# Optimization experiments

Hardware: AMD Instinct MI355X
Metric: run time of the kernel (lower is better)

The kernel has to match this reference:

```python
import jax, jax.numpy as jnp
import numpy as np

REL, DIM = 8, 256
B, S, T = 8, 512, 512


def setup_inputs() -> dict:
    key = jax.random.key(0)
    k = jax.random.split(key, 8)
    return {
        "src_emb": jax.random.normal(k[0], (B, S, DIM), jnp.float32),
        "tar_emb": jax.random.normal(k[1], (B, T, DIM), jnp.float32),
        "src_mask": jnp.ones((B, S), jnp.float32),
        "tar_mask": jnp.ones((B, T), jnp.float32),
        "mul_score_w": jax.random.normal(k[2], (REL, DIM, DIM), jnp.float32) * 0.05,
        "mul_emb_w": jax.random.normal(k[3], (REL, DIM, DIM), jnp.float32) * 0.05,
        "src_none_node": jax.random.normal(k[4], (DIM,), jnp.float32),
        "tar_none_node": jax.random.normal(k[5], (DIM,), jnp.float32),
    }


def reference(src_emb, tar_emb, src_mask, tar_mask,
              mul_score_w, mul_emb_w, src_none_node, tar_none_node):
    b = src_emb.shape[0]
    dim = src_emb.shape[2]
    rel = mul_score_w.shape[0]
    ones = jnp.ones((b, 1), src_mask.dtype)
    # append learned 'none' node to both src and tar (always unmasked)
    src_mask_ = jnp.concatenate([src_mask, ones], axis=1)            # [b, S+1]
    src_emb_ = jnp.concatenate(
        [src_emb, jnp.broadcast_to(src_none_node[None, None, :], (b, 1, dim))], axis=1)
    tar_mask_ = jnp.concatenate([tar_mask, ones], axis=1)            # [b, T+1]
    tar_emb_ = jnp.concatenate(
        [tar_emb, jnp.broadcast_to(tar_none_node[None, None, :], (b, 1, dim))], axis=1)

    # per-relation projected src: [rel, b, S+1, dim]
    scores = jnp.einsum('bsd,rde->rbse', src_emb_, mul_score_w)
    # relation-wise bilinear scores: [rel, b, S+1, T+1]
    st = jnp.einsum('rbse,bte->rbst', scores, tar_emb_)
    pair_mask = src_mask_[:, :, None] * tar_mask_[:, None, :]        # [b, S+1, T+1]
    st = (st + (1.0 - pair_mask)[None] * (-1e10)) * (1.0 / np.sqrt(dim))
    # softmax over the SRC axis (softmax_src=True)
    w = jax.nn.softmax(st, axis=2)                                   # [rel, b, S+1, T+1]

    # per-relation projected tar: [rel, b, T+1, dim]
    rel_tar = jnp.einsum('btd,rde->rbte', tar_emb_, mul_emb_w)
    # use_tar_node=False: drop appended tar none-node from both factors
    rel_tar = rel_tar[:, :, :-1, :]                                  # [rel, b, T, dim]
    w = w[:, :, :, :-1]                                              # [rel, b, S+1, T]

    # tar_sum=True, use_normalize=False: sum over tar then rel, scaled by 1/sqrt(rel)
    mul_emb = jnp.einsum('rbst,rbtd->bsd', w, rel_tar) * (1.0 / np.sqrt(rel))
    # src_none_node present: drop appended src row
    return mul_emb[:, :-1, :]                                        # [b, S, dim]
```

## Files before the change

### kernel.cpp

```cpp
#include <hip/hip_runtime.h>

#define RELN 8
#define DIMN 256
#define BN_  8
#define SN   512
#define TN   512

typedef __attribute__((ext_vector_type(8))) short bf16x8;
typedef __attribute__((ext_vector_type(4))) short bf16x4;
typedef __attribute__((ext_vector_type(4))) float f32x4;

__device__ __forceinline__ unsigned short f2bf(float f) {
    union { float f; unsigned u; } x; x.f = f;
    return (unsigned short)((x.u + 0x7FFFu + ((x.u >> 16) & 1u)) >> 16);
}
__device__ __forceinline__ float bf2f(unsigned short h) {
    union { unsigned u; float f; } x; x.u = (unsigned)h << 16; return x.f;
}

#define TBM 128
#define TBN 128
#define TBK 64
#define BP  132

template<int MODE>
__global__ __launch_bounds__(256, 2)
void gemm_bt(const unsigned short* __restrict__ A,
             const unsigned short* __restrict__ B,
             void* __restrict__ C, int K, int lda, int ldb,
             const float* __restrict__ msrc,
             const float* __restrict__ mtar,
             float* __restrict__ Lsum)
{
    __shared__ unsigned short Sh[2][2][TBM * TBK];
    const int tid  = threadIdx.x;
    const int lane = tid & 63;
    const int wv   = tid >> 6;
    const int wr   = (wv >> 1) * 64;
    const int wc   = (wv & 1) * 64;
    const int m0   = blockIdx.x * TBM;
    const int n0   = blockIdx.y * TBN;
    const int z    = blockIdx.z;
    const int bblk = m0 >> 9;
    const int rz   = z * 2;

    const unsigned short* Ab = A;
    const unsigned short* Bb = B;
    if (MODE == 1)      { Bb += (size_t)z * DIMN * DIMN; }
    else if (MODE == 2) { Ab += (size_t)z * SN * DIMN; Bb += (size_t)(z & 7) * TN * DIMN; }
    else if (MODE == 3) { Bb += (size_t)z * DIMN * DIMN; }

    auto stage = [&](int buf, int kt) {
        #pragma unroll
        for (int p = 0; p < 4; ++p) {
            int idx8 = p * 256 + tid;
            int row  = idx8 >> 3;
            int col  = (idx8 & 7) << 3;
            size_t aoff, boff;
            if (MODE == 4) {
                int r = rz + (kt >> 9);
                int t = (kt & 511) + col;
                aoff = ((size_t)((r*BN_ + bblk)*SN + ((m0 + row) & 511)))*TN + t;
                boff = ((size_t)((r*BN_ + bblk)*DIMN + (n0 + row)))*TN + t;
            } else {
                aoff = (size_t)(m0 + row)*lda + kt + col;
                boff = (size_t)(n0 + row)*ldb + kt + col;
            }
            __builtin_amdgcn_global_load_lds(
                (const __attribute__((address_space(1))) unsigned int*)&Ab[aoff],
                (__attribute__((address_space(3))) unsigned int*)
                    &Sh[buf][0][p*2048 + wv*512], 16, 0, 0);
            __builtin_amdgcn_global_load_lds(
                (const __attribute__((address_space(1))) unsigned int*)&Bb[boff],
                (__attribute__((address_space(3))) unsigned int*)
                    &Sh[buf][1][p*2048 + wv*512], 16, 0, 0);
        }
    };

    f32x4 acc[4][4] = {};
    const int nsteps = K / TBK;
    stage(0, 0);
    int cur = 0;
    for (int s = 0; s < nsteps; ++s) {
        __syncthreads();
        if (s + 1 < nsteps) stage(cur ^ 1, (s + 1) * TBK);
        const unsigned short* As = Sh[cur][0];
        const unsigned short* Bs = Sh[cur][1];
        #pragma unroll
        for (int kk = 0; kk < 2; ++kk) {
            const int ko = kk*32 + (lane >> 4) * 8;
            bf16x8 af[4], bfv[4];
            #pragma unroll
            for (int i = 0; i < 4; ++i)
                af[i] = *(const bf16x8*)&As[(wr + i*16 + (lane & 15))*TBK + ko];
            #pragma unroll
            for (int j = 0; j < 4; ++j)
                bfv[j] = *(const bf16x8*)&Bs[(wc + j*16 + (lane & 15))*TBK + ko];
            #pragma unroll
            for (int i = 0; i < 4; ++i) {
                #pragma unroll
                for (int j = 0; j < 4; ++j)
                    acc[i][j] = __builtin_amdgcn_mfma_f32_16x16x32_bf16(af[i], bfv[j], acc[i][j], 0, 0, 0);
            }
        }
        cur ^= 1;
    }

    const int r0 = (lane >> 4) * 4;
    const int cl = lane & 15;
    unsigned short* tile = &Sh[0][0][0];

    if (MODE == 2) {
        unsigned short* Cp = (unsigned short*)C + (size_t)z * SN * TN;
        const int b = z & 7;
        float tm[4];
        #pragma unroll
        for (int j = 0; j < 4; ++j) tm[j] = mtar[b*TN + n0 + wc + j*16 + cl];
        float colsum[4] = {0.f, 0.f, 0.f, 0.f};
        __syncthreads();
        #pragma unroll
        for (int i = 0; i < 4; ++i) {
            int rowl = wr + i*16 + r0;
            float sm[4];
            #pragma unroll
            for (int q = 0; q < 4; ++q) sm[q] = msrc[b*SN + m0 + rowl + q];
            #pragma unroll
            for (int j = 0; j < 4; ++j) {
                int coll = wc + j*16 + cl;
                #pragma unroll
                for (int q = 0; q < 4; ++q) {
                    float v = (acc[i][j][q] + (1.f - sm[q]*tm[j]) * -1e10f) * 0.0625f;
                    float e = __expf(v);
                    tile[(rowl + q)*BP + coll] = f2bf(e);
                    colsum[j] += e;
                }
            }
        }
        #pragma unroll
        for (int j = 0; j < 4; ++j) {
            float v = colsum[j];
            v += __shfl_xor(v, 16, 64);
            v += __shfl_xor(v, 32, 64);
            if (lane < 16)
                atomicAdd(&Lsum[(size_t)z*TN + n0 + wc + j*16 + cl], v);
        }
        __syncthreads();
        #pragma unroll
        for (int p = 0; p < 8; ++p) {
            int chunk = p * 256 + tid;
            int row = chunk >> 4, col = (chunk & 15) * 8;
            bf16x8 v = *(const bf16x8*)&tile[row*BP + col];
            *(bf16x8*)&Cp[(size_t)(m0 + row)*TN + n0 + col] = v;
        }
    } else if (MODE == 1) {
        unsigned short* Cp = (unsigned short*)C + (size_t)z * (BN_*SN) * DIMN;
        __syncthreads();
        #pragma unroll
        for (int i = 0; i < 4; ++i) {
            int rowl = wr + i*16 + r0;
            #pragma unroll
            for (int j = 0; j < 4; ++j) {
                int coll = wc + j*16 + cl;
                #pragma unroll
                for (int q = 0; q < 4; ++q)
                    tile[(rowl + q)*BP + coll] = f2bf(acc[i][j][q]);
            }
        }
        __syncthreads();
        #pragma unroll
        for (int p = 0; p < 8; ++p) {
            int chunk = p * 256 + tid;
            int row = chunk >> 4, col = (chunk & 15) * 8;
            bf16x8 v = *(const bf16x8*)&tile[row*BP + col];
            *(bf16x8*)&Cp[(size_t)(m0 + row)*DIMN + n0 + col] = v;
        }
    } else if (MODE == 3) {
        unsigned short* Cp = (unsigned short*)C;
        #pragma unroll
        for (int i = 0; i < 4; ++i) {
            int mrow = m0 + wr + i*16 + r0;
            int b = mrow >> 9, t = mrow & 511;
            float4 Lv = *(const float4*)&Lsum[((size_t)(z*BN_ + b))*TN + t];
            float inv0 = 1.f / Lv.x, inv1 = 1.f / Lv.y,
                  inv2 = 1.f / Lv.z, inv3 = 1.f / Lv.w;
            #pragma unroll
            for (int j = 0; j < 4; ++j) {
                int e = n0 + wc + j*16 + cl;
                bf16x4 v;
                v[0] = (short)f2bf(acc[i][j][0] * inv0);
                v[1] = (short)f2bf(acc[i][j][1] * inv1);
                v[2] = (short)f2bf(acc[i][j][2] * inv2);
                v[3] = (short)f2bf(acc[i][j][3] * inv3);
                *(bf16x4*)&Cp[((size_t)(z*BN_ + b)*DIMN + e)*TN + t] = v;
            }
        }
    } else {
        float* Cp = (float*)C + (size_t)z * (BN_*SN) * DIMN;
        #pragma unroll
        for (int i = 0; i < 4; ++i) {
            int row = m0 + wr + i*16 + r0;
            #pragma unroll
            for (int j = 0; j < 4; ++j) {
                int col = n0 + wc + j*16 + cl;
                #pragma unroll
                for (int q = 0; q < 4; ++q)
                    Cp[(size_t)(row + q)*DIMN + col] = acc[i][j][q];
            }
        }
    }
}

__global__ void reduce4_kernel(const float* __restrict__ part,
                               float* __restrict__ out, int n4)
{
    int i = blockIdx.x * 256 + threadIdx.x;
    if (i < n4) {
        float4 s = {0.f, 0.f, 0.f, 0.f};
        #pragma unroll
        for (int r = 0; r < 4; ++r) {
            float4 v = *(const float4*)&part[(size_t)r*(BN_*SN*DIMN) + i*4];
            s.x += v.x; s.y += v.y; s.z += v.z; s.w += v.w;
        }
        const float k = 0.35355339059327373f;
        float4 o = {s.x*k, s.y*k, s.z*k, s.w*k};
        *(float4*)&out[i*4] = o;
    }
}

__global__ void cvt2_kernel(const float* __restrict__ src,
                            const float* __restrict__ tar,
                            unsigned short* __restrict__ src_bf,
                            unsigned short* __restrict__ tar_bf)
{
    int bid = blockIdx.x;
    const float* in = (bid < 1024) ? src : tar;
    unsigned short* out = (bid < 1024) ? src_bf : tar_bf;
    int i = ((bid & 1023) * 256 + threadIdx.x) * 4;
    float4 v = *(const float4*)(in + i);
    bf16x4 o;
    o[0] = (short)f2bf(v.x); o[1] = (short)f2bf(v.y);
    o[2] = (short)f2bf(v.z); o[3] = (short)f2bf(v.w);
    *(bf16x4*)(out + i) = o;
}

__global__ void wtrans2_kernel(const float* __restrict__ wsc,
                               const float* __restrict__ wem,
                               unsigned short* __restrict__ wscT,
                               unsigned short* __restrict__ wembT)
{
    __shared__ float tile[32][33];
    int r = blockIdx.z & 7;
    const float* w = (blockIdx.z < 8) ? wsc : wem;
    unsigned short* wt = (blockIdx.z < 8) ? wscT : wembT;
    int e0 = blockIdx.x * 32, d0 = blockIdx.y * 32;
    int tx = threadIdx.x & 31, ty = threadIdx.x >> 5;
    #pragma unroll
    for (int k = 0; k < 32; k += 8)
        tile[ty + k][tx] = w[((size_t)r*DIMN + d0 + ty + k)*DIMN + e0 + tx];
    __syncthreads();
    #pragma unroll
    for (int k = 0; k < 32; k += 8)
        wt[((size_t)r*DIMN + e0 + ty + k)*DIMN + d0 + tx] = f2bf(tile[tx][ty + k]);
}

__global__ void initL_kernel(const float* __restrict__ wsc,
                             const float* __restrict__ none,
                             const unsigned short* __restrict__ tar_bf,
                             const float* __restrict__ tar_mask,
                             float* __restrict__ L)
{
    __shared__ float sn[DIMN];
    __shared__ float part[256];
    int rb = blockIdx.x, r = rb >> 3, b = rb & 7;
    {
        int e = threadIdx.x;
        float acc = 0.f;
        for (int d = 0; d < DIMN; ++d)
            acc += none[d] * wsc[((size_t)r*DIMN + d)*DIMN + e];
        sn[e] = acc;
    }
    __syncthreads();
    int tl = threadIdx.x & 127, half = threadIdx.x >> 7;
    int t = blockIdx.y * 128 + tl;
    const unsigned short* rowp = tar_bf + ((size_t)b*TN + t)*DIMN + half*128;
    float acc = 0.f;
    #pragma unroll
    for (int k = 0; k < 16; ++k) {
        bf16x8 v = *(const bf16x8*)&rowp[k*8];
        #pragma unroll
        for (int j = 0; j < 8; ++j)
            acc += bf2f((unsigned short)v[j]) * sn[half*128 + k*8 + j];
    }
    part[threadIdx.x] = acc;
    __syncthreads();
    if (half == 0) {
        float s = part[tl] + part[tl + 128];
        float tm = tar_mask[b*TN + t];
        L[(size_t)rb*TN + t] = __expf((s + (1.f - tm) * -1e10f) * 0.0625f);
    }
}

extern "C" void kernel_launch(void* const* d_in, const int* in_sizes, int n_in,
                              void* d_out, int out_size, void* d_ws, size_t ws_size,
                              hipStream_t stream)
{
    const float* src_emb  = (const float*)d_in[0];
    const float* tar_emb  = (const float*)d_in[1];
    const float* src_mask = (const float*)d_in[2];
    const float* tar_mask = (const float*)d_in[3];
    const float* w_score  = (const float*)d_in[4];
    const float* w_emb    = (const float*)d_in[5];
    const float* src_none = (const float*)d_in[6];

    size_t off = 0;
    auto alloc = [&](size_t bytes) {
        char* q = (char*)d_ws + off;
        off += (bytes + 255) & ~(size_t)255;
        return q;
    };
    unsigned short* src_bf  = (unsigned short*)alloc((size_t)BN_*SN*DIMN*2);
    unsigned short* tar_bf  = (unsigned short*)alloc((size_t)BN_*TN*DIMN*2);
    unsigned short* wscT    = (unsigned short*)alloc((size_t)RELN*DIMN*DIMN*2);
    unsigned short* wembT   = (unsigned short*)alloc((size_t)RELN*DIMN*DIMN*2);
    unsigned short* scores  = (unsigned short*)alloc((size_t)RELN*BN_*SN*DIMN*2);
    unsigned short* wbuf    = (unsigned short*)alloc((size_t)RELN*BN_*SN*TN*2);
    unsigned short* relT    = (unsigned short*)alloc((size_t)RELN*BN_*DIMN*TN*2);
    float*          outp4   = (float*)alloc((size_t)4*BN_*SN*DIMN*4);
    float*          Lsum    = (float*)alloc((size_t)RELN*BN_*TN*4);
    if (off > ws_size) return;

    cvt2_kernel<<<2048, 256, 0, stream>>>(src_emb, tar_emb, src_bf, tar_bf);
    wtrans2_kernel<<<dim3(8,8,16), 256, 0, stream>>>(w_score, w_emb, wscT, wembT);
    initL_kernel<<<dim3(64, 4), 256, 0, stream>>>(w_score, src_none, tar_bf,
                                                  tar_mask, Lsum);
    gemm_bt<1><<<dim3(32, 2, 8), 256, 0, stream>>>(src_bf, wscT, scores, DIMN, DIMN, DIMN,
                                                   nullptr, nullptr, nullptr);
    gemm_bt<2><<<dim3(4, 4, 64), 256, 0, stream>>>(scores, tar_bf, wbuf, DIMN, DIMN, DIMN,
                                                   src_mask, tar_mask, Lsum);
    gemm_bt<3><<<dim3(32, 2, 8), 256, 0, stream>>>(tar_bf, wembT, relT, DIMN, DIMN, DIMN,
                                                   nullptr, nullptr, Lsum);
    gemm_bt<4><<<dim3(32, 2, 4), 256, 0, stream>>>(wbuf, relT, outp4, 1024, 0, 0,
                                                   nullptr, nullptr, nullptr);
    reduce4_kernel<<<1024, 256, 0, stream>>>(outp4, (float*)d_out, BN_*SN*DIMN/4);
}
```

Baseline: 94.59 us.

## Template GEMM M-tile, shrink final GEMM tile, stage MODE3 stores, fuse prep kernels

Makes the GEMM M-tile size a template parameter. The final wbuf×relT GEMM now uses 64-row tiles with a 3-blocks-per-CU launch bound, which doubles its grid from 256 to 512 blocks for better CU occupancy. The MODE 3 epilogue, which writes the transposed relT, now goes through an LDS tile so global stores are coalesced 16-byte chunks instead of scattered 8-byte ones. The bf16 conversion and weight-transpose kernels are merged into one launch. The trade-off is less data reuse per block in the last GEMM.

```diff
diff --git a/kernel.cpp b/kernel.cpp
--- a/kernel.cpp
+++ b/kernel.cpp
@@ -18,27 +18,28 @@
     union { unsigned u; float f; } x; x.u = (unsigned)h << 16; return x.f;
 }
 
-#define TBM 128
 #define TBN 128
 #define TBK 64
-#define BP  132
-
-template<int MODE>
-__global__ __launch_bounds__(256, 2)
+#define BP  136
+
+template<int MODE, int BM>
+__global__ __launch_bounds__(256, (MODE == 4 ? 3 : 2))
 void gemm_bt(const unsigned short* __restrict__ A,
              const unsigned short* __restrict__ B,
-             void* __restrict__ C, int K, int lda, int ldb,
+             void* __restrict__ C, int K,
+             int lda, int ldb,
              const float* __restrict__ msrc,
              const float* __restrict__ mtar,
              float* __restrict__ Lsum)
 {
-    __shared__ unsigned short Sh[2][2][TBM * TBK];
+    constexpr int NI = BM / 32;
+    __shared__ unsigned short Sh[2][(BM + TBN) * TBK];
     const int tid  = threadIdx.x;
     const int lane = tid & 63;
     const int wv   = tid >> 6;
-    const int wr   = (wv >> 1) * 64;
+    const int wr   = (wv >> 1) * (BM / 2);
     const int wc   = (wv & 1) * 64;
-    const int m0   = blockIdx.x * TBM;
+    const int m0   = blockIdx.x * BM;
     const int n0   = blockIdx.y * TBN;
     const int z    = blockIdx.z;
     const int bblk = m0 >> 9;
@@ -51,53 +52,67 @@
     else if (MODE == 3) { Bb += (size_t)z * DIMN * DIMN; }
 
     auto stage = [&](int buf, int kt) {
+        unsigned short* Abase = Sh[buf];
+        unsigned short* Bbase = Sh[buf] + BM * TBK;
+        #pragma unroll
+        for (int p = 0; p < BM / 32; ++p) {
+            int idx8 = p * 256 + tid;
+            int row  = idx8 >> 3;
+            int col  = (idx8 & 7) << 3;
+            size_t aoff;
+            if (MODE == 4) {
+                int r = rz + (kt >> 9);
+                int t = (kt & 511) + col;
+                aoff = ((size_t)((r*BN_ + bblk)*SN + ((m0 + row) & 511)))*TN + t;
+            } else {
+                aoff = (size_t)(m0 + row)*lda + kt + col;
+            }
+            __builtin_amdgcn_global_load_lds(
+                (const __attribute__((address_space(1))) unsigned int*)&Ab[aoff],
+                (__attribute__((address_space(3))) unsigned int*)
+                    &Abase[p*2048 + wv*512], 16, 0, 0);
+        }
         #pragma unroll
         for (int p = 0; p < 4; ++p) {
             int idx8 = p * 256 + tid;
             int row  = idx8 >> 3;
             int col  = (idx8 & 7) << 3;
-            size_t aoff, boff;
+            size_t boff;
             if (MODE == 4) {
                 int r = rz + (kt >> 9);
                 int t = (kt & 511) + col;
-                aoff = ((size_t)((r*BN_ + bblk)*SN + ((m0 + row) & 511)))*TN + t;
                 boff = ((size_t)((r*BN_ + bblk)*DIMN + (n0 + row)))*TN + t;
             } else {
-                aoff = (size_t)(m0 + row)*lda + kt + col;
                 boff = (size_t)(n0 + row)*ldb + kt + col;
             }
-            __builtin_amdgcn_global_load_lds(
-                (const __attribute__((address_space(1))) unsigned int*)&Ab[aoff],
-                (__attribute__((address_space(3))) unsigned int*)
-                    &Sh[buf][0][p*2048 + wv*512], 16, 0, 0);
             __builtin_amdgcn_global_load_lds(
                 (const __attribute__((address_space(1))) unsigned int*)&Bb[boff],
                 (__attribute__((address_space(3))) unsigned int*)
-                    &Sh[buf][1][p*2048 + wv*512], 16, 0, 0);
+                    &Bbase[p*2048 + wv*512], 16, 0, 0);
         }
     };
 
-    f32x4 acc[4][4] = {};
+    f32x4 acc[NI][4] = {};
     const int nsteps = K / TBK;
     stage(0, 0);
     int cur = 0;
     for (int s = 0; s < nsteps; ++s) {
         __syncthreads();
         if (s + 1 < nsteps) stage(cur ^ 1, (s + 1) * TBK);
-        const unsigned short* As = Sh[cur][0];
-        const unsigned short* Bs = Sh[cur][1];
+        const unsigned short* As = Sh[cur];
+        const unsigned short* Bs = Sh[cur] + BM * TBK;
         #pragma unroll
         for (int kk = 0; kk < 2; ++kk) {
             const int ko = kk*32 + (lane >> 4) * 8;
-            bf16x8 af[4], bfv[4];
-            #pragma unroll
-            for (int i = 0; i < 4; ++i)
+            bf16x8 af[NI], bfv[4];
+            #pragma unroll
+            for (int i = 0; i < NI; ++i)
                 af[i] = *(const bf16x8*)&As[(wr + i*16 + (lane & 15))*TBK + ko];
             #pragma unroll
             for (int j = 0; j < 4; ++j)
                 bfv[j] = *(const bf16x8*)&Bs[(wc + j*16 + (lane & 15))*TBK + ko];
             #pragma unroll
-            for (int i = 0; i < 4; ++i) {
+            for (int i = 0; i < NI; ++i) {
                 #pragma unroll
                 for (int j = 0; j < 4; ++j)
                     acc[i][j] = __builtin_amdgcn_mfma_f32_16x16x32_bf16(af[i], bfv[j], acc[i][j], 0, 0, 0);
@@ -108,7 +123,7 @@
 
     const int r0 = (lane >> 4) * 4;
     const int cl = lane & 15;
-    unsigned short* tile = &Sh[0][0][0];
+    unsigned short* tile = &Sh[0][0];
 
     if (MODE == 2) {
         unsigned short* Cp = (unsigned short*)C + (size_t)z * SN * TN;
@@ -119,7 +134,7 @@
         float colsum[4] = {0.f, 0.f, 0.f, 0.f};
         __syncthreads();
         #pragma unroll
-        for (int i = 0; i < 4; ++i) {
+        for (int i = 0; i < NI; ++i) {
             int rowl = wr + i*16 + r0;
             float sm[4];
             #pragma unroll
@@ -156,7 +171,7 @@
         unsigned short* Cp = (unsigned short*)C + (size_t)z * (BN_*SN) * DIMN;
         __syncthreads();
         #pragma unroll
-        for (int i = 0; i < 4; ++i) {
+        for (int i = 0; i < NI; ++i) {
             int rowl = wr + i*16 + r0;
             #pragma unroll
             for (int j = 0; j < 4; ++j) {
@@ -176,28 +191,37 @@
         }
     } else if (MODE == 3) {
         unsigned short* Cp = (unsigned short*)C;
-        #pragma unroll
-        for (int i = 0; i < 4; ++i) {
-            int mrow = m0 + wr + i*16 + r0;
-            int b = mrow >> 9, t = mrow & 511;
-            float4 Lv = *(const float4*)&Lsum[((size_t)(z*BN_ + b))*TN + t];
+        const int t_base = m0 & 511;
+        __syncthreads();
+        #pragma unroll
+        for (int i = 0; i < NI; ++i) {
+            int tl0  = wr + i*16 + r0;
+            float4 Lv = *(const float4*)&Lsum[((size_t)(z*BN_ + bblk))*TN + t_base + tl0];
             float inv0 = 1.f / Lv.x, inv1 = 1.f / Lv.y,
                   inv2 = 1.f / Lv.z, inv3 = 1.f / Lv.w;
             #pragma unroll
             for (int j = 0; j < 4; ++j) {
-                int e = n0 + wc + j*16 + cl;
+                int el = wc + j*16 + cl;
                 bf16x4 v;
                 v[0] = (short)f2bf(acc[i][j][0] * inv0);
                 v[1] = (short)f2bf(acc[i][j][1] * inv1);
                 v[2] = (short)f2bf(acc[i][j][2] * inv2);
                 v[3] = (short)f2bf(acc[i][j][3] * inv3);
-                *(bf16x4*)&Cp[((size_t)(z*BN_ + b)*DIMN + e)*TN + t] = v;
-            }
+                *(bf16x4*)&tile[el*BP + tl0] = v;
+            }
+        }
+        __syncthreads();
+        #pragma unroll
+        for (int p = 0; p < 8; ++p) {
+            int chunk = p * 256 + tid;
+            int er = chunk >> 4, tc = (chunk & 15) * 8;
+            bf16x8 v = *(const bf16x8*)&tile[er*BP + tc];
+            *(bf16x8*)&Cp[((size_t)(z*BN_ + bblk)*DIMN + n0 + er)*TN + t_base + tc] = v;
         }
     } else {
         float* Cp = (float*)C + (size_t)z * (BN_*SN) * DIMN;
         #pragma unroll
-        for (int i = 0; i < 4; ++i) {
+        for (int i = 0; i < NI; ++i) {
             int row = m0 + wr + i*16 + r0;
             #pragma unroll
             for (int j = 0; j < 4; ++j) {
@@ -227,40 +251,41 @@
     }
 }
 
-__global__ void cvt2_kernel(const float* __restrict__ src,
+__global__ void prep_kernel(const float* __restrict__ src,
                             const float* __restrict__ tar,
+                            const float* __restrict__ wsc,
+                            const float* __restrict__ wem,
                             unsigned short* __restrict__ src_bf,
-                            unsigned short* __restrict__ tar_bf)
+                            unsigned short* __restrict__ tar_bf,
+                            unsigned short* __restrict__ wscT,
+                            unsigned short* __restrict__ wembT)
 {
     int bid = blockIdx.x;
-    const float* in = (bid < 1024) ? src : tar;
-    unsigned short* out = (bid < 1024) ? src_bf : tar_bf;
-    int i = ((bid & 1023) * 256 + threadIdx.x) * 4;
-    float4 v = *(const float4*)(in + i);
-    bf16x4 o;
-    o[0] = (short)f2bf(v.x); o[1] = (short)f2bf(v.y);
-    o[2] = (short)f2bf(v.z); o[3] = (short)f2bf(v.w);
-    *(bf16x4*)(out + i) = o;
-}
-
-__global__ void wtrans2_kernel(const float* __restrict__ wsc,
-                               const float* __restrict__ wem,
-                               unsigned short* __restrict__ wscT,
-                               unsigned short* __restrict__ wembT)
-{
-    __shared__ float tile[32][33];
-    int r = blockIdx.z & 7;
-    const float* w = (blockIdx.z < 8) ? wsc : wem;
-    unsigned short* wt = (blockIdx.z < 8) ? wscT : wembT;
-    int e0 = blockIdx.x * 32, d0 = blockIdx.y * 32;
-    int tx = threadIdx.x & 31, ty = threadIdx.x >> 5;
-    #pragma unroll
-    for (int k = 0; k < 32; k += 8)
-        tile[ty + k][tx] = w[((size_t)r*DIMN + d0 + ty + k)*DIMN + e0 + tx];
-    __syncthreads();
-    #pragma unroll
-    for (int k = 0; k < 32; k += 8)
-        wt[((size_t)r*DIMN + e0 + ty + k)*DIMN + d0 + tx] = f2bf(tile[tx][ty + k]);
+    if (bid < 2048) {
+        const float* in = (bid < 1024) ? src : tar;
+        unsigned short* out = (bid < 1024) ? src_bf : tar_bf;
+        int i = ((bid & 1023) * 256 + threadIdx.x) * 4;
+        float4 v = *(const float4*)(in + i);
+        bf16x4 o;
+        o[0] = (short)f2bf(v.x); o[1] = (short)f2bf(v.y);
+        o[2] = (short)f2bf(v.z); o[3] = (short)f2bf(v.w);
+        *(bf16x4*)(out + i) = o;
+    } else {
+        __shared__ float tile[32][33];
+        int b2 = bid - 2048;
+        int e0 = (b2 & 7) * 32, d0 = ((b2 >> 3) & 7) * 32, zz = b2 >> 6;
+        int r = zz & 7;
+        const float* w = (zz < 8) ? wsc : wem;
+        unsigned short* wt = (zz < 8) ? wscT : wembT;
+        int tx = threadIdx.x & 31, ty = threadIdx.x >> 5;
+        #pragma unroll
+        for (int k = 0; k < 32; k += 8)
+            tile[ty + k][tx] = w[((size_t)r*DIMN + d0 + ty + k)*DIMN + e0 + tx];
+        __syncthreads();
+        #pragma unroll
+        for (int k = 0; k < 32; k += 8)
+            wt[((size_t)r*DIMN + e0 + ty + k)*DIMN + d0 + tx] = f2bf(tile[tx][ty + k]);
+    }
 }
 
 __global__ void initL_kernel(const float* __restrict__ wsc,
@@ -329,17 +354,21 @@
     float*          Lsum    = (float*)alloc((size_t)RELN*BN_*TN*4);
     if (off > ws_size) return;
 
-    cvt2_kernel<<<2048, 256, 0, stream>>>(src_emb, tar_emb, src_bf, tar_bf);
-    wtrans2_kernel<<<dim3(8,8,16), 256, 0, stream>>>(w_score, w_emb, wscT, wembT);
+    prep_kernel<<<3072, 256, 0, stream>>>(src_emb, tar_emb, w_score, w_emb,
+                                          src_bf, tar_bf, wscT, wembT);
     initL_kernel<<<dim3(64, 4), 256, 0, stream>>>(w_score, src_none, tar_bf,
                                                   tar_mask, Lsum);
-    gemm_bt<1><<<dim3(32, 2, 8), 256, 0, stream>>>(src_bf, wscT, scores, DIMN, DIMN, DIMN,
-                                                   nullptr, nullptr, nullptr);
-    gemm_bt<2><<<dim3(4, 4, 64), 256, 0, stream>>>(scores, tar_bf, wbuf, DIMN, DIMN, DIMN,
-                                                   src_mask, tar_mask, Lsum);
-    gemm_bt<3><<<dim3(32, 2, 8), 256, 0, stream>>>(tar_bf, wembT, relT, DIMN, DIMN, DIMN,
-                                                   nullptr, nullptr, Lsum);
-    gemm_bt<4><<<dim3(32, 2, 4), 256, 0, stream>>>(wbuf, relT, outp4, 1024, 0, 0,
-                                                   nullptr, nullptr, nullptr);
+    gemm_bt<1,128><<<dim3(32, 2, 8), 256, 0, stream>>>(src_bf, wscT, scores,
+                                                       DIMN, DIMN, DIMN,
+                                                       nullptr, nullptr, nullptr);
+    gemm_bt<2,128><<<dim3(4, 4, 64), 256, 0, stream>>>(scores, tar_bf, wbuf,
+                                                       DIMN, DIMN, DIMN,
+                                                       src_mask, tar_mask, Lsum);
+    gemm_bt<3,128><<<dim3(32, 2, 8), 256, 0, stream>>>(tar_bf, wembT, relT,
+                                                       DIMN, DIMN, DIMN,
+                                                       nullptr, nullptr, Lsum);
+    gemm_bt<4,64><<<dim3(64, 2, 4), 256, 0, stream>>>(wbuf, relT, outp4,
+                                                      1024, 0, 0,
+                                                      nullptr, nullptr, nullptr);
     reduce4_kernel<<<1024, 256, 0, stream>>>(outp4, (float*)d_out, BN_*SN*DIMN/4);
 }
```

Result: no change. 96.22 us (+1.7%).
